# Kernel optimization log

Measured on AMD Instinct MI355X. Metric: run time of the kernel, lower is better.

The kernel has to match this reference:

```python
import jax, jax.numpy as jnp
import numpy as np

N_NODES = 100000
N_EDGES = 1600000
INPUT_DIM = 128
HIDDEN = 128
OUTPUT_DIM = 2
NUM_LAYERS = 2
MAX_RECURSION = 10
TAU_THRESHOLD = 0.005


def setup_inputs() -> dict:
    key = jax.random.key(0)
    ks = jax.random.split(key, 16)
    s = 0.05
    x = jax.random.normal(ks[0], (N_NODES, INPUT_DIM), dtype=jnp.float32)
    edge_index = jax.random.randint(ks[1], (2, N_EDGES), 0, N_NODES, dtype=jnp.int64)
    W_in = jax.random.normal(ks[2], (HIDDEN, INPUT_DIM), dtype=jnp.float32) * s
    b_in = jax.random.normal(ks[3], (HIDDEN,), dtype=jnp.float32) * s
    Wd = jax.random.normal(ks[4], (NUM_LAYERS, HIDDEN, 2 * HIDDEN), dtype=jnp.float32) * s
    bd = jax.random.normal(ks[5], (NUM_LAYERS, HIDDEN), dtype=jnp.float32) * s
    Wt = jax.random.normal(ks[6], (1, HIDDEN), dtype=jnp.float32) * s
    bt = jax.random.normal(ks[7], (1,), dtype=jnp.float32) * s
    W_ih = jax.random.normal(ks[8], (3 * HIDDEN, HIDDEN), dtype=jnp.float32) * s
    W_hh = jax.random.normal(ks[9], (3 * HIDDEN, HIDDEN), dtype=jnp.float32) * s
    b_ih = jax.random.normal(ks[10], (3 * HIDDEN,), dtype=jnp.float32) * s
    b_hh = jax.random.normal(ks[11], (3 * HIDDEN,), dtype=jnp.float32) * s
    Wo = jax.random.normal(ks[12], (OUTPUT_DIM, HIDDEN), dtype=jnp.float32) * s
    bo = jax.random.normal(ks[13], (OUTPUT_DIM,), dtype=jnp.float32) * s
    return dict(x=x, edge_index=edge_index, W_in=W_in, b_in=b_in, Wd=Wd, bd=bd,
                Wt=Wt, bt=bt, W_ih=W_ih, W_hh=W_hh, b_ih=b_ih, b_hh=b_hh, Wo=Wo, bo=bo)


def _gru_cell(x, h, W_ih, W_hh, b_ih, b_hh):
    # torch.nn.GRUCell math
    gi = x @ W_ih.T + b_ih  # [N, 3H]
    gh = h @ W_hh.T + b_hh
    i_r, i_z, i_n = jnp.split(gi, 3, axis=-1)
    h_r, h_z, h_n = jnp.split(gh, 3, axis=-1)
    r = jax.nn.sigmoid(i_r + h_r)
    z = jax.nn.sigmoid(i_z + h_z)
    n = jnp.tanh(i_n + r * h_n)
    return (1.0 - z) * n + z * h


def reference(x, edge_index, W_in, b_in, Wd, bd, Wt, bt, W_ih, W_hh, b_ih, b_hh, Wo, bo):
    N = x.shape[0]
    row, col = edge_index[0], edge_index[1]
    h = jax.nn.relu(x @ W_in.T + b_in)  # [N, H]
    tau = None
    for l in range(NUM_LAYERS):
        diff = jnp.abs(h[row] - h[col])  # [E, H]
        diff_agg = jax.ops.segment_sum(diff, row, num_segments=N)  # [N, H]
        h = jax.nn.relu(jnp.concatenate([h, diff_agg], axis=-1) @ Wd[l].T + bd[l])
        tau = jax.nn.softplus(h @ Wt.T + bt).squeeze(-1)  # [N]
        # n_updates = clamp(floor(1/tau), max=MAX_RECURSION); node updated iff
        # n_updates > 0 and tau < TAU_THRESHOLD. The original inner loop applies
        # gru(diff_agg[i], h[i]) with the ORIGINAL h[i] each iteration, so repeated
        # application is idempotent -> single masked GRU step is exact same math.
        n_updates = jnp.minimum(jnp.floor(1.0 / tau).astype(jnp.int32), MAX_RECURSION)
        mask = (n_updates > 0) & (tau < TAU_THRESHOLD)
        h_gru = _gru_cell(diff_agg, h, W_ih, W_hh, b_ih, b_hh)
        h = jnp.where(mask[:, None], h_gru, h)
    out = h @ Wo.T + bo  # [N, OUTPUT_DIM]
    return out, tau
```

## Files before the change

### kernel.cpp

```cpp
#include <hip/hip_runtime.h>
#include <cstdint>
#include <cstddef>

#define HID 128
#define BSHIFT 7
#define NSB 256
#define MAXB 4096

__global__ __launch_bounds__(256)
void transpose_all_kernel(const float* __restrict__ W_in, const float* __restrict__ Wd,
                          const float* __restrict__ W_ih, const float* __restrict__ W_hh,
                          float* __restrict__ WinT, float* __restrict__ WdT0,
                          float* __restrict__ WdT1, float* __restrict__ WihT,
                          float* __restrict__ WhhT) {
  int i = blockIdx.x * 256 + threadIdx.x;
  if (i < 16384) { int r = i >> 7, c = i & 127; WinT[c * 128 + r] = W_in[i]; return; }
  i -= 16384;
  if (i < 32768) { int r = i >> 8, c = i & 255; WdT0[c * 128 + r] = Wd[i]; return; }
  i -= 32768;
  if (i < 32768) { int r = i >> 8, c = i & 255; WdT1[c * 128 + r] = Wd[32768 + i]; return; }
  i -= 32768;
  if (i < 49152) { int r = i >> 7, c = i & 127; WihT[c * 384 + r] = W_ih[i]; return; }
  i -= 49152;
  if (i < 49152) { int r = i >> 7, c = i & 127; WhhT[c * 384 + r] = W_hh[i]; }
}

__global__ __launch_bounds__(256)
void ecount_kernel(const int* __restrict__ row, int* __restrict__ countsT,
                   int E, int nbuck) {
  __shared__ int lh[1024];
  int b = blockIdx.x;
  for (int i = threadIdx.x; i < nbuck; i += 256) lh[i] = 0;
  __syncthreads();
  int per = (E + NSB - 1) / NSB;
  int s = b * per, e = min(s + per, E);
  for (int i = s + (int)threadIdx.x; i < e; i += 256)
    atomicAdd(&lh[row[i] >> BSHIFT], 1);
  __syncthreads();
  for (int i = threadIdx.x; i < nbuck; i += 256) countsT[i * NSB + b] = lh[i];
}

__global__ __launch_bounds__(NSB)
void bprefix_kernel(int* __restrict__ countsT, int* __restrict__ btotal, int nbuck) {
  __shared__ int sd[NSB];
  int bk = blockIdx.x;
  int t = threadIdx.x;
  int v = countsT[bk * NSB + t];
  sd[t] = v;
  __syncthreads();
  for (int off = 1; off < NSB; off <<= 1) {
    int u = (t >= off) ? sd[t - off] : 0;
    __syncthreads();
    sd[t] += u;
    __syncthreads();
  }
  countsT[bk * NSB + t] = sd[t] - v;
  if (t == NSB - 1) btotal[bk] = sd[t];
}

__global__ __launch_bounds__(1024)
void bstart_kernel(const int* __restrict__ btotal, int* __restrict__ bstart,
                   int* __restrict__ offsets, int N, int nbuck) {
  __shared__ int sd[1024];
  int t = threadIdx.x;
  int v = (t < nbuck) ? btotal[t] : 0;
  sd[t] = v;
  __syncthreads();
  for (int off = 1; off < 1024; off <<= 1) {
    int u = (t >= off) ? sd[t - off] : 0;
    __syncthreads();
    sd[t] += u;
    __syncthreads();
  }
  if (t < nbuck) bstart[t] = sd[t] - v;
  if (t == nbuck - 1) { bstart[nbuck] = sd[t]; offsets[N] = sd[t]; }
}

__global__ __launch_bounds__(256)
void escatter_kernel(const int* __restrict__ row, const int* __restrict__ col,
                     const int* __restrict__ countsT, const int* __restrict__ bstart,
                     int2* __restrict__ ebuf, int E, int nbuck) {
  __shared__ int lcur[1024];
  int b = blockIdx.x;
  for (int i = threadIdx.x; i < nbuck; i += 256)
    lcur[i] = bstart[i] + countsT[i * NSB + b];
  __syncthreads();
  int per = (E + NSB - 1) / NSB;
  int s = b * per, e = min(s + per, E);
  for (int i = s + (int)threadIdx.x; i < e; i += 256) {
    int r = row[i], c = col[i];
    int pos = atomicAdd(&lcur[r >> BSHIFT], 1);
    ebuf[pos] = make_int2(r, c);
  }
}

__global__ __launch_bounds__(256)
void bsort_kernel(const int2* __restrict__ ebuf, const int* __restrict__ bstart,
                  int* __restrict__ offsets, int* __restrict__ csr_col,
                  int N, int nbuck) {
  __shared__ int cnt[128], off[128], cur[128];
  __shared__ int lcol[MAXB];
  int bk = blockIdx.x;
  int tid = threadIdx.x;
  int s = bstart[bk], e = bstart[bk + 1];
  int m = e - s;
  if (tid < 128) cnt[tid] = 0;
  __syncthreads();
  for (int i = s + tid; i < e; i += 256)
    atomicAdd(&cnt[ebuf[i].x & 127], 1);
  __syncthreads();
  if (tid < 128) off[tid] = cnt[tid];
  __syncthreads();
  for (int d = 1; d < 128; d <<= 1) {
    int v = 0;
    if (tid < 128 && tid >= d) v = off[tid - d];
    __syncthreads();
    if (tid < 128) off[tid] += v;
    __syncthreads();
  }
  if (tid < 128) {
    cur[tid] = off[tid] - cnt[tid];
    int node = (bk << BSHIFT) + tid;
    if (node < N) offsets[node] = s + off[tid] - cnt[tid];
  }
  __syncthreads();
  if (m <= MAXB) {
    for (int i = s + tid; i < e; i += 256) {
      int2 rc = ebuf[i];
      int pos = atomicAdd(&cur[rc.x & 127], 1);
      lcol[pos] = rc.y;
    }
    __syncthreads();
    if (tid < 128) {
      int b0 = off[tid] - cnt[tid], b1 = off[tid];
      for (int i = b0 + 1; i < b1; ++i) {
        int key = lcol[i];
        int j = i - 1;
        while (j >= b0 && lcol[j] > key) { lcol[j + 1] = lcol[j]; --j; }
        lcol[j + 1] = key;
      }
    }
    __syncthreads();
    for (int i = tid; i < m; i += 256) csr_col[s + i] = lcol[i];
  } else {
    for (int i = s + tid; i < e; i += 256) {
      int2 rc = ebuf[i];
      int pos = atomicAdd(&cur[rc.x & 127], 1);
      csr_col[s + pos] = rc.y;
    }
  }
}

__global__ __launch_bounds__(256)
void aggregate_kernel(const float* __restrict__ h, const int* __restrict__ offsets,
                      const int* __restrict__ csr_col, float* __restrict__ diff,
                      int N) {
  int wave = threadIdx.x >> 6;
  int lane = threadIdx.x & 63;
  int node = blockIdx.x * 4 + wave;
  if (node >= N) return;
  int start = offsets[node], end = offsets[node + 1];
  int deg = end - start;
  const float2* hrow = (const float2*)(h + (size_t)node * HID);
  float2 hv = hrow[lane];
  float a0 = 0.f, a1 = 0.f;

  int batch = min(deg, 64);
  int myc = (lane < batch) ? csr_col[start + lane] : 0;
  int j = 0;
  for (; j + 8 <= batch; j += 8) {
    const float2* p0 = (const float2*)(h + (size_t)__shfl(myc, j + 0) * HID);
    const float2* p1 = (const float2*)(h + (size_t)__shfl(myc, j + 1) * HID);
    const float2* p2 = (const float2*)(h + (size_t)__shfl(myc, j + 2) * HID);
    const float2* p3 = (const float2*)(h + (size_t)__shfl(myc, j + 3) * HID);
    const float2* p4 = (const float2*)(h + (size_t)__shfl(myc, j + 4) * HID);
    const float2* p5 = (const float2*)(h + (size_t)__shfl(myc, j + 5) * HID);
    const float2* p6 = (const float2*)(h + (size_t)__shfl(myc, j + 6) * HID);
    const float2* p7 = (const float2*)(h + (size_t)__shfl(myc, j + 7) * HID);
    float2 x0 = p0[lane], x1 = p1[lane], x2 = p2[lane], x3 = p3[lane];
    float2 x4 = p4[lane], x5 = p5[lane], x6 = p6[lane], x7 = p7[lane];
    a0 += fabsf(hv.x - x0.x) + fabsf(hv.x - x1.x) + fabsf(hv.x - x2.x) + fabsf(hv.x - x3.x)
        + fabsf(hv.x - x4.x) + fabsf(hv.x - x5.x) + fabsf(hv.x - x6.x) + fabsf(hv.x - x7.x);
    a1 += fabsf(hv.y - x0.y) + fabsf(hv.y - x1.y) + fabsf(hv.y - x2.y) + fabsf(hv.y - x3.y)
        + fabsf(hv.y - x4.y) + fabsf(hv.y - x5.y) + fabsf(hv.y - x6.y) + fabsf(hv.y - x7.y);
  }
  for (; j < batch; ++j) {
    const float2* p = (const float2*)(h + (size_t)__shfl(myc, j) * HID);
    float2 x = p[lane];
    a0 += fabsf(hv.x - x.x);
    a1 += fabsf(hv.y - x.y);
  }
  for (int e = start + 64; e < end; ++e) {
    const float2* p = (const float2*)(h + (size_t)csr_col[e] * HID);
    float2 x = p[lane];
    a0 += fabsf(hv.x - x.x);
    a1 += fabsf(hv.y - x.y);
  }
  *(float2*)(diff + (size_t)node * HID + 2 * lane) = make_float2(a0, a1);
}

template<bool TAU>
__global__ __launch_bounds__(512)
void gemm_kernel(const float* __restrict__ A1, const float* __restrict__ A2,
                 const float* __restrict__ BT, const float* __restrict__ bias,
                 float* __restrict__ C, int M, int nchunks,
                 const float* __restrict__ Wt, const float* __restrict__ bt,
                 float* __restrict__ tau_out, int* __restrict__ mlist,
                 int* __restrict__ mcount) {
  __shared__ float As[32][132];
  __shared__ float Bs[32][128];
  __shared__ float taured[128];
  int tid = threadIdx.x;
  int tx = tid & 31;
  int ty = tid >> 5;
  int i0 = blockIdx.x * 128;
  float acc[8][4] = {};

  for (int kc = 0; kc < nchunks; ++kc) {
    const float* A = (kc < 4) ? A1 : A2;
    int ksrc = (kc & 3) * 32;
    int kglob = kc * 32;
    #pragma unroll
    for (int q = 0; q < 2; ++q) {
      int f = q * 512 + tid;
      int i = f >> 3;
      int kq = (f & 7) << 2;
      int ig = i0 + i; if (ig >= M) ig = M - 1;
      float4 v = *(const float4*)(A + (size_t)ig * HID + ksrc + kq);
      As[kq + 0][i] = v.x; As[kq + 1][i] = v.y;
      As[kq + 2][i] = v.z; As[kq + 3][i] = v.w;
    }
    #pragma unroll
    for (int q = 0; q < 2; ++q) {
      int f = q * 512 + tid;
      int k = f >> 5; int c4 = (f & 31) << 2;
      *(float4*)&Bs[k][c4] = *(const float4*)(BT + (size_t)(kglob + k) * HID + c4);
    }
    __syncthreads();
    #pragma unroll
    for (int k = 0; k < 32; ++k) {
      float a[8], b[4];
      const float4* ap = (const float4*)&As[k][ty * 8];
      float4 a0 = ap[0], a1 = ap[1];
      a[0]=a0.x; a[1]=a0.y; a[2]=a0.z; a[3]=a0.w;
      a[4]=a1.x; a[5]=a1.y; a[6]=a1.z; a[7]=a1.w;
      #pragma unroll
      for (int u = 0; u < 4; ++u) b[u] = Bs[k][tx + 32 * u];
      #pragma unroll
      for (int r = 0; r < 8; ++r)
        #pragma unroll
        for (int u = 0; u < 4; ++u)
          acc[r][u] = fmaf(a[r], b[u], acc[r][u]);
    }
    __syncthreads();
  }

  float bias_r[4], wt_r[4];
  #pragma unroll
  for (int u = 0; u < 4; ++u) { bias_r[u] = bias[tx + 32 * u]; wt_r[u] = 0.f; }
  if constexpr (TAU) {
    #pragma unroll
    for (int u = 0; u < 4; ++u) wt_r[u] = Wt[tx + 32 * u];
  }
  #pragma unroll
  for (int r = 0; r < 8; ++r) {
    int row = i0 + ty * 8 + r;
    bool ok = row < M;
    float p = 0.f;
    #pragma unroll
    for (int u = 0; u < 4; ++u) {
      float v = fmaxf(acc[r][u] + bias_r[u], 0.f);
      if (ok) C[(size_t)row * HID + tx + 32 * u] = v;
      p = fmaf(v, wt_r[u], p);
    }
    if constexpr (TAU) {
      p += __shfl_down(p, 16, 32);
      p += __shfl_down(p, 8, 32);
      p += __shfl_down(p, 4, 32);
      p += __shfl_down(p, 2, 32);
      p += __shfl_down(p, 1, 32);
      if (tx == 0) taured[ty * 8 + r] = p;
    }
  }
  if constexpr (TAU) {
    __syncthreads();
    if (tid < 128) {
      int row = i0 + tid;
      if (row < M) {
        float pre = taured[tid] + bt[0];
        float tau = (pre > 20.f) ? pre : log1pf(expf(pre));
        tau_out[row] = tau;
        if (tau < 0.005f && (1.0f / tau) < 2147483648.0f) {
          int pos = atomicAdd(mcount, 1);
          mlist[pos] = row;
        }
      }
    }
  }
}

__global__ __launch_bounds__(512)
void gru_kernel(const float* __restrict__ diff, float* __restrict__ h,
                const int* __restrict__ list, const int* __restrict__ count,
                const float* __restrict__ WihT, const float* __restrict__ WhhT,
                const float* __restrict__ b_ih, const float* __restrict__ b_hh) {
  int cnt = *count;
  int base = blockIdx.x * 32;
  if (base >= cnt) return;
  __shared__ float dl[32][HID];
  __shared__ float hl[32][HID];
  __shared__ int ids[32];
  int tid = threadIdx.x;
  if (tid < 32) ids[tid] = (base + tid < cnt) ? list[base + tid] : -1;
  __syncthreads();
  #pragma unroll
  for (int q = 0; q < 8; ++q) {
    int f = q * 512 + tid;
    int r = f >> 7, c = f & 127;
    int id = ids[r];
    int src = (id >= 0) ? id : 0;
    dl[r][c] = diff[(size_t)src * HID + c];
    hl[r][c] = h[(size_t)src * HID + c];
  }
  __syncthreads();
  int tx = tid & 127, ty = tid >> 7;
  float air[8] = {}, aiz[8] = {}, ain[8] = {}, ahr[8] = {}, ahz[8] = {}, ahn[8] = {};
  for (int k = 0; k < HID; ++k) {
    float wir = WihT[k * 384 + tx];
    float wiz = WihT[k * 384 + 128 + tx];
    float win = WihT[k * 384 + 256 + tx];
    float whr = WhhT[k * 384 + tx];
    float whz = WhhT[k * 384 + 128 + tx];
    float whn = WhhT[k * 384 + 256 + tx];
    #pragma unroll
    for (int r = 0; r < 8; ++r) {
      float dk = dl[ty * 8 + r][k];
      float hk = hl[ty * 8 + r][k];
      air[r] = fmaf(dk, wir, air[r]);
      aiz[r] = fmaf(dk, wiz, aiz[r]);
      ain[r] = fmaf(dk, win, ain[r]);
      ahr[r] = fmaf(hk, whr, ahr[r]);
      ahz[r] = fmaf(hk, whz, ahz[r]);
      ahn[r] = fmaf(hk, whn, ahn[r]);
    }
  }
  float bir = b_ih[tx], biz = b_ih[128 + tx], bin = b_ih[256 + tx];
  float bhr = b_hh[tx], bhz = b_hh[128 + tx], bhn = b_hh[256 + tx];
  #pragma unroll
  for (int r = 0; r < 8; ++r) {
    int id = ids[ty * 8 + r];
    if (id < 0) continue;
    float rg = 1.f / (1.f + expf(-((air[r] + bir) + (ahr[r] + bhr))));
    float z  = 1.f / (1.f + expf(-((aiz[r] + biz) + (ahz[r] + bhz))));
    float n  = tanhf((ain[r] + bin) + rg * (ahn[r] + bhn));
    float hv = hl[ty * 8 + r][tx];
    h[(size_t)id * HID + tx] = (1.f - z) * n + z * hv;
  }
}

__global__ void out_kernel(const float* __restrict__ h, const float* __restrict__ Wo,
                           const float* __restrict__ bo, float* __restrict__ out, int N) {
  int g = blockIdx.x * blockDim.x + threadIdx.x;
  int node = g >> 6;
  int lane = threadIdx.x & 63;
  if (node >= N) return;
  float h0 = h[(size_t)node * HID + lane];
  float h1 = h[(size_t)node * HID + 64 + lane];
  float s0 = h0 * Wo[lane] + h1 * Wo[64 + lane];
  float s1 = h0 * Wo[128 + lane] + h1 * Wo[192 + lane];
  for (int d = 32; d; d >>= 1) {
    s0 += __shfl_down(s0, d);
    s1 += __shfl_down(s1, d);
  }
  if (lane == 0) {
    out[(size_t)node * 2 + 0] = s0 + bo[0];
    out[(size_t)node * 2 + 1] = s1 + bo[1];
  }
}

extern "C" void kernel_launch(void* const* d_in, const int* in_sizes, int n_in,
                              void* d_out, int out_size, void* d_ws, size_t ws_size,
                              hipStream_t stream) {
  const float* x    = (const float*)d_in[0];
  const int*   ei   = (const int*)d_in[1];
  const float* W_in = (const float*)d_in[2];
  const float* b_in = (const float*)d_in[3];
  const float* Wd   = (const float*)d_in[4];
  const float* bd   = (const float*)d_in[5];
  const float* Wt   = (const float*)d_in[6];
  const float* bt   = (const float*)d_in[7];
  const float* W_ih = (const float*)d_in[8];
  const float* W_hh = (const float*)d_in[9];
  const float* b_ih = (const float*)d_in[10];
  const float* b_hh = (const float*)d_in[11];
  const float* Wo   = (const float*)d_in[12];
  const float* bo   = (const float*)d_in[13];

  const int N = in_sizes[0] / HID;
  const int E = in_sizes[1] / 2;
  const int* rowp = ei;
  const int* colp = ei + E;
  const int nbuck = (N + (1 << BSHIFT) - 1) >> BSHIFT;

  char* p = (char*)d_ws;
  auto alloc = [&](size_t bytes) { void* r = (void*)p; p += (bytes + 255) & ~(size_t)255; return r; };
  float* hA     = (float*)alloc((size_t)N * HID * 4);
  float* hB     = (float*)alloc((size_t)N * HID * 4);
  float* diff   = (float*)alloc((size_t)N * HID * 4);
  float* WinT   = (float*)alloc(128 * 128 * 4);
  float* WdT0   = (float*)alloc(256 * 128 * 4);
  float* WdT1   = (float*)alloc(256 * 128 * 4);
  float* WihT   = (float*)alloc(128 * 384 * 4);
  float* WhhT   = (float*)alloc(128 * 384 * 4);
  float* tau0   = (float*)alloc((size_t)N * 4);
  int*   list   = (int*)alloc((size_t)N * 4);
  int*   count  = (int*)alloc(256);
  int*   countsT= (int*)alloc((size_t)1024 * NSB * 4);
  int*   btotal = (int*)alloc(1024 * 4);
  int*   bstart = (int*)alloc(1028 * 4);
  int*   offs   = (int*)alloc(((size_t)N + 1) * 4);
  int*   csrcol = (int*)alloc((size_t)E * 4);
  int2*  ebuf   = (int2*)alloc((size_t)E * 8);

  float* out_ptr = (float*)d_out;
  float* tau_out = (float*)d_out + (size_t)N * 2;

  hipMemsetAsync(count, 0, 8, stream);

  transpose_all_kernel<<<(180224 + 255) / 256, 256, 0, stream>>>(
      W_in, Wd, W_ih, W_hh, WinT, WdT0, WdT1, WihT, WhhT);

  ecount_kernel<<<NSB, 256, 0, stream>>>(rowp, countsT, E, nbuck);
  bprefix_kernel<<<nbuck, NSB, 0, stream>>>(countsT, btotal, nbuck);
  bstart_kernel<<<1, 1024, 0, stream>>>(btotal, bstart, offs, N, nbuck);
  escatter_kernel<<<NSB, 256, 0, stream>>>(rowp, colp, countsT, bstart, ebuf, E, nbuck);
  bsort_kernel<<<nbuck, 256, 0, stream>>>(ebuf, bstart, offs, csrcol, N, nbuck);

  const int gemm_blocks = (N + 127) / 128;
  const int agg_blocks = (N + 3) / 4;
  const int gru_blocks = (N + 31) / 32;

  gemm_kernel<false><<<gemm_blocks, 512, 0, stream>>>(
      x, nullptr, WinT, b_in, hA, N, 4, nullptr, nullptr, nullptr, nullptr, nullptr);

  aggregate_kernel<<<agg_blocks, 256, 0, stream>>>(hA, offs, csrcol, diff, N);
  gemm_kernel<true><<<gemm_blocks, 512, 0, stream>>>(
      hA, diff, WdT0, bd, hB, N, 8, Wt, bt, tau0, list, count);
  gru_kernel<<<gru_blocks, 512, 0, stream>>>(diff, hB, list, count, WihT, WhhT, b_ih, b_hh);

  aggregate_kernel<<<agg_blocks, 256, 0, stream>>>(hB, offs, csrcol, diff, N);
  gemm_kernel<true><<<gemm_blocks, 512, 0, stream>>>(
      hB, diff, WdT1, bd + 128, hA, N, 8, Wt, bt, tau_out, list, count + 1);
  gru_kernel<<<gru_blocks, 512, 0, stream>>>(diff, hA, list, count + 1, WihT, WhhT, b_ih, b_hh);

  out_kernel<<<((size_t)N * 64 + 255) / 256, 256, 0, stream>>>(hA, Wo, bo, out_ptr, N);
}
```

Baseline: 781.1 us.

## Fold weight transpose into ecount, unroll aggregation by 16, vectorize output head

Merges the weight-transpose kernel into the edge-count kernel using a grid-stride loop, which removes one kernel launch. Adds a 16-way unrolled gather loop in the aggregation kernel so more neighbor rows are in flight per wave. Rewrites the output projection to use 32 lanes per node with float4 loads, halving the thread count and the shuffle-reduction depth. The extra unroll raises register pressure in the aggregation kernel, which may lower occupancy.

```diff
diff --git a/kernel.cpp b/kernel.cpp
--- a/kernel.cpp
+++ b/kernel.cpp
@@ -8,26 +8,25 @@
 #define MAXB 4096
 
 __global__ __launch_bounds__(256)
-void transpose_all_kernel(const float* __restrict__ W_in, const float* __restrict__ Wd,
-                          const float* __restrict__ W_ih, const float* __restrict__ W_hh,
-                          float* __restrict__ WinT, float* __restrict__ WdT0,
-                          float* __restrict__ WdT1, float* __restrict__ WihT,
-                          float* __restrict__ WhhT) {
-  int i = blockIdx.x * 256 + threadIdx.x;
-  if (i < 16384) { int r = i >> 7, c = i & 127; WinT[c * 128 + r] = W_in[i]; return; }
-  i -= 16384;
-  if (i < 32768) { int r = i >> 8, c = i & 255; WdT0[c * 128 + r] = Wd[i]; return; }
-  i -= 32768;
-  if (i < 32768) { int r = i >> 8, c = i & 255; WdT1[c * 128 + r] = Wd[32768 + i]; return; }
-  i -= 32768;
-  if (i < 49152) { int r = i >> 7, c = i & 127; WihT[c * 384 + r] = W_ih[i]; return; }
-  i -= 49152;
-  if (i < 49152) { int r = i >> 7, c = i & 127; WhhT[c * 384 + r] = W_hh[i]; }
-}
-
-__global__ __launch_bounds__(256)
 void ecount_kernel(const int* __restrict__ row, int* __restrict__ countsT,
-                   int E, int nbuck) {
+                   int E, int nbuck,
+                   const float* __restrict__ W_in, const float* __restrict__ Wd,
+                   const float* __restrict__ W_ih, const float* __restrict__ W_hh,
+                   float* __restrict__ WinT, float* __restrict__ WdT0,
+                   float* __restrict__ WdT1, float* __restrict__ WihT,
+                   float* __restrict__ WhhT) {
+  for (int i = blockIdx.x * 256 + threadIdx.x; i < 180224; i += NSB * 256) {
+    int j = i;
+    if (j < 16384) { int r = j >> 7, c = j & 127; WinT[c * 128 + r] = W_in[j]; continue; }
+    j -= 16384;
+    if (j < 32768) { int r = j >> 8, c = j & 255; WdT0[c * 128 + r] = Wd[j]; continue; }
+    j -= 32768;
+    if (j < 32768) { int r = j >> 8, c = j & 255; WdT1[c * 128 + r] = Wd[32768 + j]; continue; }
+    j -= 32768;
+    if (j < 49152) { int r = j >> 7, c = j & 127; WihT[c * 384 + r] = W_ih[j]; continue; }
+    j -= 49152;
+    { int r = j >> 7, c = j & 127; WhhT[c * 384 + r] = W_hh[j]; }
+  }
   __shared__ int lh[1024];
   int b = blockIdx.x;
   for (int i = threadIdx.x; i < nbuck; i += 256) lh[i] = 0;
@@ -168,6 +167,36 @@
   int batch = min(deg, 64);
   int myc = (lane < batch) ? csr_col[start + lane] : 0;
   int j = 0;
+  for (; j + 16 <= batch; j += 16) {
+    const float2* p0 = (const float2*)(h + (size_t)__shfl(myc, j + 0) * HID);
+    const float2* p1 = (const float2*)(h + (size_t)__shfl(myc, j + 1) * HID);
+    const float2* p2 = (const float2*)(h + (size_t)__shfl(myc, j + 2) * HID);
+    const float2* p3 = (const float2*)(h + (size_t)__shfl(myc, j + 3) * HID);
+    const float2* p4 = (const float2*)(h + (size_t)__shfl(myc, j + 4) * HID);
+    const float2* p5 = (const float2*)(h + (size_t)__shfl(myc, j + 5) * HID);
+    const float2* p6 = (const float2*)(h + (size_t)__shfl(myc, j + 6) * HID);
+    const float2* p7 = (const float2*)(h + (size_t)__shfl(myc, j + 7) * HID);
+    const float2* q0 = (const float2*)(h + (size_t)__shfl(myc, j + 8) * HID);
+    const float2* q1 = (const float2*)(h + (size_t)__shfl(myc, j + 9) * HID);
+    const float2* q2 = (const float2*)(h + (size_t)__shfl(myc, j + 10) * HID);
+    const float2* q3 = (const float2*)(h + (size_t)__shfl(myc, j + 11) * HID);
+    const float2* q4 = (const float2*)(h + (size_t)__shfl(myc, j + 12) * HID);
+    const float2* q5 = (const float2*)(h + (size_t)__shfl(myc, j + 13) * HID);
+    const float2* q6 = (const float2*)(h + (size_t)__shfl(myc, j + 14) * HID);
+    const float2* q7 = (const float2*)(h + (size_t)__shfl(myc, j + 15) * HID);
+    float2 x0 = p0[lane], x1 = p1[lane], x2 = p2[lane], x3 = p3[lane];
+    float2 x4 = p4[lane], x5 = p5[lane], x6 = p6[lane], x7 = p7[lane];
+    float2 y0 = q0[lane], y1 = q1[lane], y2 = q2[lane], y3 = q3[lane];
+    float2 y4 = q4[lane], y5 = q5[lane], y6 = q6[lane], y7 = q7[lane];
+    a0 += fabsf(hv.x - x0.x) + fabsf(hv.x - x1.x) + fabsf(hv.x - x2.x) + fabsf(hv.x - x3.x)
+        + fabsf(hv.x - x4.x) + fabsf(hv.x - x5.x) + fabsf(hv.x - x6.x) + fabsf(hv.x - x7.x);
+    a1 += fabsf(hv.y - x0.y) + fabsf(hv.y - x1.y) + fabsf(hv.y - x2.y) + fabsf(hv.y - x3.y)
+        + fabsf(hv.y - x4.y) + fabsf(hv.y - x5.y) + fabsf(hv.y - x6.y) + fabsf(hv.y - x7.y);
+    a0 += fabsf(hv.x - y0.x) + fabsf(hv.x - y1.x) + fabsf(hv.x - y2.x) + fabsf(hv.x - y3.x)
+        + fabsf(hv.x - y4.x) + fabsf(hv.x - y5.x) + fabsf(hv.x - y6.x) + fabsf(hv.x - y7.x);
+    a1 += fabsf(hv.y - y0.y) + fabsf(hv.y - y1.y) + fabsf(hv.y - y2.y) + fabsf(hv.y - y3.y)
+        + fabsf(hv.y - y4.y) + fabsf(hv.y - y5.y) + fabsf(hv.y - y6.y) + fabsf(hv.y - y7.y);
+  }
   for (; j + 8 <= batch; j += 8) {
     const float2* p0 = (const float2*)(h + (size_t)__shfl(myc, j + 0) * HID);
     const float2* p1 = (const float2*)(h + (size_t)__shfl(myc, j + 1) * HID);
@@ -361,18 +390,19 @@
 __global__ void out_kernel(const float* __restrict__ h, const float* __restrict__ Wo,
                            const float* __restrict__ bo, float* __restrict__ out, int N) {
   int g = blockIdx.x * blockDim.x + threadIdx.x;
-  int node = g >> 6;
-  int lane = threadIdx.x & 63;
+  int node = g >> 5;
+  int sub = threadIdx.x & 31;
   if (node >= N) return;
-  float h0 = h[(size_t)node * HID + lane];
-  float h1 = h[(size_t)node * HID + 64 + lane];
-  float s0 = h0 * Wo[lane] + h1 * Wo[64 + lane];
-  float s1 = h0 * Wo[128 + lane] + h1 * Wo[192 + lane];
-  for (int d = 32; d; d >>= 1) {
-    s0 += __shfl_down(s0, d);
-    s1 += __shfl_down(s1, d);
-  }
-  if (lane == 0) {
+  float4 hv = *(const float4*)(h + (size_t)node * HID + sub * 4);
+  float4 w0 = *(const float4*)(Wo + sub * 4);
+  float4 w1 = *(const float4*)(Wo + 128 + sub * 4);
+  float s0 = hv.x * w0.x + hv.y * w0.y + hv.z * w0.z + hv.w * w0.w;
+  float s1 = hv.x * w1.x + hv.y * w1.y + hv.z * w1.z + hv.w * w1.w;
+  for (int d = 16; d; d >>= 1) {
+    s0 += __shfl_down(s0, d, 32);
+    s1 += __shfl_down(s1, d, 32);
+  }
+  if (sub == 0) {
     out[(size_t)node * 2 + 0] = s0 + bo[0];
     out[(size_t)node * 2 + 1] = s1 + bo[1];
   }
@@ -427,10 +457,9 @@
 
   hipMemsetAsync(count, 0, 8, stream);
 
-  transpose_all_kernel<<<(180224 + 255) / 256, 256, 0, stream>>>(
-      W_in, Wd, W_ih, W_hh, WinT, WdT0, WdT1, WihT, WhhT);
-
-  ecount_kernel<<<NSB, 256, 0, stream>>>(rowp, countsT, E, nbuck);
+  ecount_kernel<<<NSB, 256, 0, stream>>>(rowp, countsT, E, nbuck,
+                                         W_in, Wd, W_ih, W_hh,
+                                         WinT, WdT0, WdT1, WihT, WhhT);
   bprefix_kernel<<<nbuck, NSB, 0, stream>>>(countsT, btotal, nbuck);
   bstart_kernel<<<1, 1024, 0, stream>>>(btotal, bstart, offs, N, nbuck);
   escatter_kernel<<<NSB, 256, 0, stream>>>(rowp, colp, countsT, bstart, ebuf, E, nbuck);
@@ -453,5 +482,5 @@
       hB, diff, WdT1, bd + 128, hA, N, 8, Wt, bt, tau_out, list, count + 1);
   gru_kernel<<<gru_blocks, 512, 0, stream>>>(diff, hA, list, count + 1, WihT, WhhT, b_ih, b_hh);
 
-  out_kernel<<<((size_t)N * 64 + 255) / 256, 256, 0, stream>>>(hA, Wo, bo, out_ptr, N);
-}
+  out_kernel<<<((size_t)N * 32 + 255) / 256, 256, 0, stream>>>(hA, Wo, bo, out_ptr, N);
+}
```

After: 764.2 us. 1.02x faster.
